# Kernel optimization log

Hardware: AMD Instinct MI355X
Metric: run time of the kernel (lower is better)

## Reference

```python
import jax, jax.numpy as jnp
import numpy as np

B, N, S, K = 16, 4, 64, 50        # batch, n_answers, q_len, n_boxes
VD, QD, H = 1024, 768, 512        # v_dim, q_dim, num_hid


def setup_inputs() -> dict:
    key = jax.random.key(0)
    ks = jax.random.split(key, 10)
    inp = {
        "v": jax.random.normal(ks[0], (B, 1, K, VD), dtype=jnp.float32),
        "q": jax.random.normal(ks[1], (B, N, S, 1, QD), dtype=jnp.float32),
        "box_mask": jax.random.randint(ks[2], (B, K), 0, 2, dtype=jnp.int32),
        "tags_attention": jax.random.normal(ks[3], (B, K), dtype=jnp.float32),
        # learned params (nn.Linear stores weight as [out, in])
        "Wv": jax.random.normal(ks[4], (H, VD), dtype=jnp.float32) * 0.02,
        "bv": jnp.zeros((H,), dtype=jnp.float32),
        "Wq": jax.random.normal(ks[5], (H, QD), dtype=jnp.float32) * 0.02,
        "bq": jnp.zeros((H,), dtype=jnp.float32),
        "Wl": jax.random.normal(ks[6], (1, H), dtype=jnp.float32) * 0.02,
        "bl": jnp.zeros((1,), dtype=jnp.float32),
    }
    return inp


def reference(v, q, box_mask, tags_attention, Wv, bv, Wq, bq, Wl, bl):
    # v_proj = Linear(v).unsqueeze(1): [B,1,K,H] -> [B,1,1,K,H]
    v_proj = (jnp.einsum('bokd,hd->bokh', v, Wv) + bv)[:, None]
    # q_proj: [B,N,S,1,H]
    q_proj = jnp.einsum('bnsod,hd->bnsoh', q, Wq) + bq
    # broadcast add + tanh: joint_repr [B,N,S,K,H] (the big intermediate)
    joint_repr = jnp.tanh(v_proj + q_proj)
    # score reduce over H: logits [B,N,S,K]
    logits = jnp.einsum('bnskh,oh->bnsko', joint_repr, Wl)[..., 0] + bl[0]
    # masked softmax over boxes with mask box_mask[:,None,None] -> [B,1,1,K]
    mask = (box_mask > 0)[:, None, None]
    w = jax.nn.softmax(jnp.where(mask, logits, jnp.float32(-1e9)), axis=-1)
    return w
```

## Files before the change

kernel.cpp:

```cpp
#include <hip/hip_runtime.h>
#include <hip/hip_bf16.h>
#include <cstddef>


typedef __attribute__((ext_vector_type(2))) float          f32x2;
typedef __attribute__((ext_vector_type(4))) float          f32x4;
typedef __attribute__((ext_vector_type(8))) short          bfrag;
typedef __attribute__((ext_vector_type(2))) unsigned int   u32x2;
typedef __attribute__((ext_vector_type(4))) unsigned short u16x4;

#define SBAR   __builtin_amdgcn_s_barrier()
#define SCHED0 __builtin_amdgcn_sched_barrier(0)

__device__ __forceinline__ void gload16(const void* g, void* l) {
  __builtin_amdgcn_global_load_lds((const __attribute__((address_space(1))) void*)g,
                                   (__attribute__((address_space(3))) void*)l, 16, 0, 0);
}

__device__ __forceinline__ unsigned int cvtpk(float a, float b) {
  unsigned int r;
  asm("v_cvt_pk_bf16_f32 %0, %1, %2" : "=v"(r) : "v"(a), "v"(b));
  return r;
}

__device__ __forceinline__ float bf2f(unsigned short u) {
  return __uint_as_float((unsigned int)u << 16);
}

template<int CTRL>
__device__ __forceinline__ float dpp_add(float x) {
  int r = __builtin_amdgcn_update_dpp(0, __float_as_int(x), CTRL, 0xF, 0xF, false);
  return x + __int_as_float(r);
}

__global__ void __launch_bounds__(256) cvt_all(
    const float* __restrict__ v, const float* __restrict__ wv,
    const float* __restrict__ q, const float* __restrict__ wq,
    unsigned short* __restrict__ vb, unsigned short* __restrict__ wvb,
    unsigned short* __restrict__ qb, unsigned short* __restrict__ wqb) {
  const int total = 1220608;
  for (int f = blockIdx.x * 256 + threadIdx.x; f < total; f += gridDim.x * 256) {
    const float* src; unsigned short* dst; int off;
    if (f < 204800)       { src = v;  dst = vb;  off = f; }
    else if (f < 335872)  { src = wv; dst = wvb; off = f - 204800; }
    else if (f < 1122304) { src = q;  dst = qb;  off = f - 335872; }
    else                  { src = wq; dst = wqb; off = f - 1122304; }
    f32x4 x = ((const f32x4*)src)[off];
    u32x2 p; p[0] = cvtpk(x[0], x[1]); p[1] = cvtpk(x[2], x[3]);
    ((u32x2*)dst)[off] = p;
  }
}

__global__ void __launch_bounds__(256) gemm_bf16(
    const unsigned short* __restrict__ vb, const unsigned short* __restrict__ qb,
    const unsigned short* __restrict__ wvb, const unsigned short* __restrict__ wqb,
    const float* __restrict__ bv, const float* __restrict__ bq,
    unsigned short* __restrict__ evw, unsigned short* __restrict__ qpw) {
  __shared__ unsigned short As[2][64 * 64];
  __shared__ unsigned short Bs[2][64 * 64];

  const int id = blockIdx.x;
  const int m  = (id & 7) + ((id >> 6) << 3);
  const int nt = (id >> 3) & 7;
  if (m >= 77) return;

  const int t = threadIdx.x;

  const unsigned short* A; const unsigned short* W; const float* bias;
  int M, Kd, m0;
  const bool vpath = (m < 13);
  if (vpath) { A = vb; W = wvb; bias = bv; M = 800;  Kd = 1024; m0 = m * 64; }
  else       { A = qb; W = wqb; bias = bq; M = 4096; Kd = 768;  m0 = (m - 13) * 64; }
  const int n0 = nt * 64;

  const int lane = t & 63;
  const int wave = t >> 6;
  const int wm   = wave >> 1;
  const int wn   = wave & 1;
  const int la   = lane & 15;
  const int lb   = lane >> 4;

  const int row1 = t >> 3;
  const int p1   = (t & 7) ^ (row1 & 7);
  int grA1 = m0 + row1;      if (grA1 >= M) grA1 = M - 1;
  int grA2 = m0 + row1 + 32; if (grA2 >= M) grA2 = M - 1;
  const unsigned short* srcA1 = A + (size_t)grA1 * Kd + p1 * 8;
  const unsigned short* srcA2 = A + (size_t)grA2 * Kd + p1 * 8;
  const unsigned short* srcB1 = W + (size_t)(n0 + row1) * Kd + p1 * 8;
  const unsigned short* srcB2 = W + (size_t)(n0 + row1 + 32) * Kd + p1 * 8;

  const int d1 = wave * 512;
  const int d2 = 2048 + wave * 512;

  auto STAGE = [&](int buf, int s) {
    const int o = s * 64;
    gload16(srcA1 + o, &As[buf][d1]);
    gload16(srcA2 + o, &As[buf][d2]);
    gload16(srcB1 + o, &Bs[buf][d1]);
    gload16(srcB2 + o, &Bs[buf][d2]);
  };

  f32x4 acc[2][2] = {};

  auto compute = [&](const unsigned short* sa, const unsigned short* sb) {
    bfrag af[2][2], bf[2][2];
#pragma unroll
    for (int r = 0; r < 2; ++r)
#pragma unroll
      for (int kk = 0; kk < 2; ++kk) {
        int rowa = wm * 32 + r * 16 + la;
        af[r][kk] = *(const bfrag*)((const char*)sa +
                     ((rowa * 128 + kk * 64 + lb * 16) ^ ((rowa & 7) << 4)));
        int rowb = wn * 32 + r * 16 + la;
        bf[r][kk] = *(const bfrag*)((const char*)sb +
                     ((rowb * 128 + kk * 64 + lb * 16) ^ ((rowb & 7) << 4)));
      }
#pragma unroll
    for (int kk = 0; kk < 2; ++kk)
#pragma unroll
      for (int r = 0; r < 2; ++r)
#pragma unroll
        for (int c = 0; c < 2; ++c)
          acc[r][c] = __builtin_amdgcn_mfma_f32_16x16x32_bf16(af[r][kk], bf[c][kk], acc[r][c], 0, 0, 0);
  };

  const int nsteps = Kd >> 6;
  STAGE(0, 0);
  STAGE(1, 1);
  for (int s = 0; s < nsteps; ++s) {
    if (s + 1 < nsteps) { asm volatile("s_waitcnt vmcnt(4)" ::: "memory"); }
    else                { asm volatile("s_waitcnt vmcnt(0)" ::: "memory"); }
    SCHED0;
    SBAR; SCHED0;
    compute(As[s & 1], Bs[s & 1]);
    SBAR; SCHED0;
    if (s + 2 < nsteps) STAGE(s & 1, s + 2);
  }

  const float CEXP = 2.885390081777927f;
  unsigned short* C = vpath ? evw : qpw;
#pragma unroll
  for (int c = 0; c < 2; ++c) {
    int col = n0 + wn * 32 + c * 16 + la;
    float bcol = bias[col];
#pragma unroll
    for (int r = 0; r < 2; ++r) {
      int mbase = m0 + wm * 32 + r * 16 + lb * 4;
#pragma unroll
      for (int e = 0; e < 4; ++e) {
        int mr = mbase + e;
        if (mr < M) {
          float val = __builtin_amdgcn_exp2f((acc[r][c][e] + bcol) * CEXP);
          C[(size_t)mr * 512 + col] = (unsigned short)cvtpk(val, val);
        }
      }
    }
  }
}

__global__ void
__attribute__((amdgpu_flat_work_group_size(512, 512), amdgpu_waves_per_eu(4, 4)))
stage3_kernel(
    const unsigned short* __restrict__ ev, const unsigned short* __restrict__ qp,
    const float* __restrict__ wl, const int* __restrict__ box_mask,
    float* __restrict__ out) {
  __shared__ unsigned short vpS[50][512];
  __shared__ float redS[8][64][8];

  const int b    = blockIdx.y;
  const int grp  = blockIdx.x;
  const int t    = threadIdx.x;
  const int wv   = t >> 6;
  const int lane = t & 63;
  const int row0 = b * 256 + grp * 16 + wv * 2;

  const unsigned short* q0 = qp + (size_t)row0 * 512;
  float eq0[8], eq1[8], wlr[8];
#pragma unroll
  for (int j = 0; j < 2; ++j) {
    u16x4 a = *(const u16x4*)&q0[j * 256 + 4 * lane];
    u16x4 c = *(const u16x4*)&q0[512 + j * 256 + 4 * lane];
    f32x4 w = *(const f32x4*)&wl[j * 256 + 4 * lane];
#pragma unroll
    for (int e = 0; e < 4; ++e) {
      eq0[j * 4 + e] = bf2f(a[e]);
      eq1[j * 4 + e] = bf2f(c[e]);
      wlr[j * 4 + e] = -2.f * w[e];
    }
  }

  {
    const unsigned short* src = ev + (size_t)b * 25600 + lane * 8;
#pragma unroll
    for (int i = 0; i < 7; ++i) {
      int kr = i * 8 + wv;
      if (kr < 50) gload16(src + kr * 512, &vpS[kr][0]);
    }
  }
  __syncthreads();

  const int g  = lane >> 4;
  const int li = lane & 15;

#pragma unroll 1
  for (int kc = 0; kc < 5; ++kc) {
    float a0[10], a1[10];
#pragma unroll
    for (int i = 0; i < 10; ++i) { a0[i] = 0.f; a1[i] = 0.f; }

#pragma unroll
    for (int i = 0; i < 10; ++i) {
      const unsigned short* vr = &vpS[kc * 10 + i][0];
      u16x4 va = *(const u16x4*)&vr[4 * lane];
      u16x4 vb2 = *(const u16x4*)&vr[256 + 4 * lane];
#pragma unroll
      for (int e = 0; e < 4; ++e) {
        float evf = bf2f(va[e]);
        a0[i] = fmaf(wlr[e], __builtin_amdgcn_rcpf(fmaf(evf, eq0[e], 1.f)), a0[i]);
        a1[i] = fmaf(wlr[e], __builtin_amdgcn_rcpf(fmaf(evf, eq1[e], 1.f)), a1[i]);
      }
#pragma unroll
      for (int e = 0; e < 4; ++e) {
        float evf = bf2f(vb2[e]);
        a0[i] = fmaf(wlr[4 + e], __builtin_amdgcn_rcpf(fmaf(evf, eq0[4 + e], 1.f)), a0[i]);
        a1[i] = fmaf(wlr[4 + e], __builtin_amdgcn_rcpf(fmaf(evf, eq1[4 + e], 1.f)), a1[i]);
      }
    }

#pragma unroll
    for (int i = 0; i < 10; ++i) {
      int k = kc * 10 + i;
      float s0 = a0[i], s1 = a1[i];
      s0 = dpp_add<0x128>(s0); s0 = dpp_add<0x124>(s0);
      s0 = dpp_add<0x122>(s0); s0 = dpp_add<0x121>(s0);
      s1 = dpp_add<0x128>(s1); s1 = dpp_add<0x124>(s1);
      s1 = dpp_add<0x122>(s1); s1 = dpp_add<0x121>(s1);
      if (li == (k & 15)) {
        f32x2 p; p[0] = s0; p[1] = s1;
        *(f32x2*)&redS[wv][k][g * 2] = p;
      }
    }
  }

  const int k = lane;
  f32x4 ra = *(const f32x4*)&redS[wv][k][0];
  f32x4 rb = *(const f32x4*)&redS[wv][k][4];
  float l0 = (ra[0] + ra[2]) + (rb[0] + rb[2]);
  float l1 = (ra[1] + ra[3]) + (rb[1] + rb[3]);

  int   msk = (k < 50) ? box_mask[b * 50 + k] : 0;
  bool  on  = (k < 50 && msk > 0);
  float L0 = on ? l0 : -1e9f;
  float L1 = on ? l1 : -1e9f;

  float m0 = L0, m1 = L1;
#pragma unroll
  for (int off = 32; off; off >>= 1) {
    m0 = fmaxf(m0, __shfl_xor(m0, off));
    m1 = fmaxf(m1, __shfl_xor(m1, off));
  }
  const float LOG2E = 1.4426950408889634f;
  float e0 = (k < 50) ? __builtin_amdgcn_exp2f((L0 - m0) * LOG2E) : 0.f;
  float e1 = (k < 50) ? __builtin_amdgcn_exp2f((L1 - m1) * LOG2E) : 0.f;
  float s0 = e0, s1 = e1;
#pragma unroll
  for (int off = 32; off; off >>= 1) {
    s0 += __shfl_xor(s0, off);
    s1 += __shfl_xor(s1, off);
  }

  if (k < 50) {
    out[(size_t)row0 * 50 + k]       = e0 / s0;
    out[(size_t)(row0 + 1) * 50 + k] = e1 / s1;
  }
}

extern "C" void kernel_launch(void* const* d_in, const int* in_sizes, int n_in,
                              void* d_out, int out_size, void* d_ws, size_t ws_size,
                              hipStream_t stream) {
  const float* v        = (const float*)d_in[0];
  const float* q        = (const float*)d_in[1];
  const int*   box_mask = (const int*)d_in[2];
  const float* Wv       = (const float*)d_in[4];
  const float* bv       = (const float*)d_in[5];
  const float* Wq       = (const float*)d_in[6];
  const float* bq       = (const float*)d_in[7];
  const float* Wl       = (const float*)d_in[8];
  float* out = (float*)d_out;

  char* ws = (char*)d_ws;
  unsigned short* qpw = (unsigned short*)(ws);
  unsigned short* evw = (unsigned short*)(ws + 4194304);
  unsigned short* vb  = (unsigned short*)(ws + 5013504);
  unsigned short* qb  = (unsigned short*)(ws + 6651904);
  unsigned short* wvb = (unsigned short*)(ws + 12943360);
  unsigned short* wqb = (unsigned short*)(ws + 13991936);

  cvt_all<<<2048, 256, 0, stream>>>(v, Wv, q, Wq, vb, wvb, qb, wqb);
  gemm_bf16<<<dim3(640), 256, 0, stream>>>(vb, qb, wvb, wqb, bv, bq, evw, qpw);
  stage3_kernel<<<dim3(16, 16), 512, 0, stream>>>(evw, qpw, Wl, box_mask, out);
}
```

Baseline: 44.77 us.

## Fuse conversion, GEMM and score stages into one cooperative persistent kernel

Replaces the three separate launches (fp32-to-bf16 conversion, bf16 GEMM, tanh-score softmax) with a single cooperative kernel of 256 blocks of 512 threads. The stages are separated by grid-wide syncs, and each block runs two GEMM tiles at once, one per 256-thread half. A subset of blocks runs an extra pair of tiles to cover all 616. This removes two kernel launch gaps and their tail idle time, at the cost of grid barrier overhead. It also introduces load imbalance in the GEMM phase and caps occupancy at 2 waves per EU.

```diff
diff --git a/kernel.cpp b/kernel.cpp
--- a/kernel.cpp
+++ b/kernel.cpp
@@ -1,6 +1,9 @@
 #include <hip/hip_runtime.h>
 #include <hip/hip_bf16.h>
+#include <hip/hip_cooperative_groups.h>
 #include <cstddef>
+
+namespace cg = cooperative_groups;
 
 
 typedef __attribute__((ext_vector_type(2))) float          f32x2;
@@ -33,38 +36,14 @@
   return x + __int_as_float(r);
 }
 
-__global__ void __launch_bounds__(256) cvt_all(
-    const float* __restrict__ v, const float* __restrict__ wv,
-    const float* __restrict__ q, const float* __restrict__ wq,
-    unsigned short* __restrict__ vb, unsigned short* __restrict__ wvb,
-    unsigned short* __restrict__ qb, unsigned short* __restrict__ wqb) {
-  const int total = 1220608;
-  for (int f = blockIdx.x * 256 + threadIdx.x; f < total; f += gridDim.x * 256) {
-    const float* src; unsigned short* dst; int off;
-    if (f < 204800)       { src = v;  dst = vb;  off = f; }
-    else if (f < 335872)  { src = wv; dst = wvb; off = f - 204800; }
-    else if (f < 1122304) { src = q;  dst = qb;  off = f - 335872; }
-    else                  { src = wq; dst = wqb; off = f - 1122304; }
-    f32x4 x = ((const f32x4*)src)[off];
-    u32x2 p; p[0] = cvtpk(x[0], x[1]); p[1] = cvtpk(x[2], x[3]);
-    ((u32x2*)dst)[off] = p;
-  }
-}
-
-__global__ void __launch_bounds__(256) gemm_bf16(
+__device__ __forceinline__ void gemm_tile(
+    int u, int t, unsigned short* AsBase, unsigned short* BsBase,
     const unsigned short* __restrict__ vb, const unsigned short* __restrict__ qb,
     const unsigned short* __restrict__ wvb, const unsigned short* __restrict__ wqb,
     const float* __restrict__ bv, const float* __restrict__ bq,
     unsigned short* __restrict__ evw, unsigned short* __restrict__ qpw) {
-  __shared__ unsigned short As[2][64 * 64];
-  __shared__ unsigned short Bs[2][64 * 64];
-
-  const int id = blockIdx.x;
-  const int m  = (id & 7) + ((id >> 6) << 3);
-  const int nt = (id >> 3) & 7;
-  if (m >= 77) return;
-
-  const int t = threadIdx.x;
+  const int m  = u >> 3;
+  const int nt = u & 7;
 
   const unsigned short* A; const unsigned short* W; const float* bias;
   int M, Kd, m0;
@@ -94,10 +73,10 @@
 
   auto STAGE = [&](int buf, int s) {
     const int o = s * 64;
-    gload16(srcA1 + o, &As[buf][d1]);
-    gload16(srcA2 + o, &As[buf][d2]);
-    gload16(srcB1 + o, &Bs[buf][d1]);
-    gload16(srcB2 + o, &Bs[buf][d2]);
+    gload16(srcA1 + o, AsBase + buf * 4096 + d1);
+    gload16(srcA2 + o, AsBase + buf * 4096 + d2);
+    gload16(srcB1 + o, BsBase + buf * 4096 + d1);
+    gload16(srcB2 + o, BsBase + buf * 4096 + d2);
   };
 
   f32x4 acc[2][2] = {};
@@ -132,7 +111,7 @@
     else                { asm volatile("s_waitcnt vmcnt(0)" ::: "memory"); }
     SCHED0;
     SBAR; SCHED0;
-    compute(As[s & 1], Bs[s & 1]);
+    compute(AsBase + (s & 1) * 4096, BsBase + (s & 1) * 4096);
     SBAR; SCHED0;
     if (s + 2 < nsteps) STAGE(s & 1, s + 2);
   }
@@ -159,119 +138,157 @@
 }
 
 __global__ void
-__attribute__((amdgpu_flat_work_group_size(512, 512), amdgpu_waves_per_eu(4, 4)))
-stage3_kernel(
-    const unsigned short* __restrict__ ev, const unsigned short* __restrict__ qp,
-    const float* __restrict__ wl, const int* __restrict__ box_mask,
-    float* __restrict__ out) {
-  __shared__ unsigned short vpS[50][512];
-  __shared__ float redS[8][64][8];
-
-  const int b    = blockIdx.y;
-  const int grp  = blockIdx.x;
-  const int t    = threadIdx.x;
-  const int wv   = t >> 6;
-  const int lane = t & 63;
-  const int row0 = b * 256 + grp * 16 + wv * 2;
-
-  const unsigned short* q0 = qp + (size_t)row0 * 512;
-  float eq0[8], eq1[8], wlr[8];
-#pragma unroll
-  for (int j = 0; j < 2; ++j) {
-    u16x4 a = *(const u16x4*)&q0[j * 256 + 4 * lane];
-    u16x4 c = *(const u16x4*)&q0[512 + j * 256 + 4 * lane];
-    f32x4 w = *(const f32x4*)&wl[j * 256 + 4 * lane];
-#pragma unroll
-    for (int e = 0; e < 4; ++e) {
-      eq0[j * 4 + e] = bf2f(a[e]);
-      eq1[j * 4 + e] = bf2f(c[e]);
-      wlr[j * 4 + e] = -2.f * w[e];
-    }
-  }
+__attribute__((amdgpu_flat_work_group_size(512, 512), amdgpu_waves_per_eu(2, 2)))
+mega(const float* __restrict__ v,  const float* __restrict__ q,
+     const int* __restrict__ box_mask,
+     const float* __restrict__ Wv, const float* __restrict__ bv,
+     const float* __restrict__ Wq, const float* __restrict__ bq,
+     const float* __restrict__ Wl, float* __restrict__ out,
+     unsigned short* qpw, unsigned short* evw,
+     unsigned short* vbuf, unsigned short* qbuf,
+     unsigned short* wvb, unsigned short* wqb) {
+  cg::grid_group grid = cg::this_grid();
+  __attribute__((aligned(16))) __shared__ char smem[67584];
+
+  const int bid = blockIdx.x;
+  const int t   = threadIdx.x;
 
   {
-    const unsigned short* src = ev + (size_t)b * 25600 + lane * 8;
-#pragma unroll
-    for (int i = 0; i < 7; ++i) {
-      int kr = i * 8 + wv;
-      if (kr < 50) gload16(src + kr * 512, &vpS[kr][0]);
-    }
-  }
-  __syncthreads();
-
-  const int g  = lane >> 4;
-  const int li = lane & 15;
+    const int total = 1220608;
+    for (int f = bid * 512 + t; f < total; f += 131072) {
+      const float* src; unsigned short* dst; int off;
+      if (f < 204800)       { src = v;  dst = vbuf; off = f; }
+      else if (f < 335872)  { src = Wv; dst = wvb;  off = f - 204800; }
+      else if (f < 1122304) { src = q;  dst = qbuf; off = f - 335872; }
+      else                  { src = Wq; dst = wqb;  off = f - 1122304; }
+      f32x4 x = ((const f32x4*)src)[off];
+      u32x2 p; p[0] = cvtpk(x[0], x[1]); p[1] = cvtpk(x[2], x[3]);
+      ((u32x2*)dst)[off] = p;
+    }
+  }
+  grid.sync();
+
+  {
+    const int sub  = t >> 8;
+    const int tsub = t & 255;
+    unsigned short* As = (unsigned short*)(smem + sub * 32768);
+    unsigned short* Bs = As + 8192;
+
+    gemm_tile(bid * 2 + sub, tsub, As, Bs, vbuf, qbuf, wvb, wqb, bv, bq, evw, qpw);
+    if (bid >= 52 && bid < 104)
+      gemm_tile(512 + (bid - 52) * 2 + sub, tsub, As, Bs, vbuf, qbuf, wvb, wqb, bv, bq, evw, qpw);
+  }
+  grid.sync();
+
+  {
+    unsigned short (*vpS)[512] = (unsigned short(*)[512])smem;
+    float (*redS)[64][8]       = (float(*)[64][8])(smem + 51200);
+
+    const int b    = bid >> 4;
+    const int grp  = bid & 15;
+    const int wv   = t >> 6;
+    const int lane = t & 63;
+    const int row0 = b * 256 + grp * 16 + wv * 2;
+
+    const unsigned short* q0 = qpw + (size_t)row0 * 512;
+    float eq0[8], eq1[8], wlr[8];
+#pragma unroll
+    for (int j = 0; j < 2; ++j) {
+      u16x4 a = *(const u16x4*)&q0[j * 256 + 4 * lane];
+      u16x4 c = *(const u16x4*)&q0[512 + j * 256 + 4 * lane];
+      f32x4 w = *(const f32x4*)&Wl[j * 256 + 4 * lane];
+#pragma unroll
+      for (int e = 0; e < 4; ++e) {
+        eq0[j * 4 + e] = bf2f(a[e]);
+        eq1[j * 4 + e] = bf2f(c[e]);
+        wlr[j * 4 + e] = -2.f * w[e];
+      }
+    }
+
+    {
+      const unsigned short* src = evw + (size_t)b * 25600 + lane * 8;
+#pragma unroll
+      for (int i = 0; i < 7; ++i) {
+        int kr = i * 8 + wv;
+        if (kr < 50) gload16(src + kr * 512, &vpS[kr][0]);
+      }
+    }
+    __syncthreads();
+
+    const int g  = lane >> 4;
+    const int li = lane & 15;
 
 #pragma unroll 1
-  for (int kc = 0; kc < 5; ++kc) {
-    float a0[10], a1[10];
-#pragma unroll
-    for (int i = 0; i < 10; ++i) { a0[i] = 0.f; a1[i] = 0.f; }
-
-#pragma unroll
-    for (int i = 0; i < 10; ++i) {
-      const unsigned short* vr = &vpS[kc * 10 + i][0];
-      u16x4 va = *(const u16x4*)&vr[4 * lane];
-      u16x4 vb2 = *(const u16x4*)&vr[256 + 4 * lane];
-#pragma unroll
-      for (int e = 0; e < 4; ++e) {
-        float evf = bf2f(va[e]);
-        a0[i] = fmaf(wlr[e], __builtin_amdgcn_rcpf(fmaf(evf, eq0[e], 1.f)), a0[i]);
-        a1[i] = fmaf(wlr[e], __builtin_amdgcn_rcpf(fmaf(evf, eq1[e], 1.f)), a1[i]);
-      }
-#pragma unroll
-      for (int e = 0; e < 4; ++e) {
-        float evf = bf2f(vb2[e]);
-        a0[i] = fmaf(wlr[4 + e], __builtin_amdgcn_rcpf(fmaf(evf, eq0[4 + e], 1.f)), a0[i]);
-        a1[i] = fmaf(wlr[4 + e], __builtin_amdgcn_rcpf(fmaf(evf, eq1[4 + e], 1.f)), a1[i]);
-      }
-    }
-
-#pragma unroll
-    for (int i = 0; i < 10; ++i) {
-      int k = kc * 10 + i;
-      float s0 = a0[i], s1 = a1[i];
-      s0 = dpp_add<0x128>(s0); s0 = dpp_add<0x124>(s0);
-      s0 = dpp_add<0x122>(s0); s0 = dpp_add<0x121>(s0);
-      s1 = dpp_add<0x128>(s1); s1 = dpp_add<0x124>(s1);
-      s1 = dpp_add<0x122>(s1); s1 = dpp_add<0x121>(s1);
-      if (li == (k & 15)) {
-        f32x2 p; p[0] = s0; p[1] = s1;
-        *(f32x2*)&redS[wv][k][g * 2] = p;
-      }
-    }
-  }
-
-  const int k = lane;
-  f32x4 ra = *(const f32x4*)&redS[wv][k][0];
-  f32x4 rb = *(const f32x4*)&redS[wv][k][4];
-  float l0 = (ra[0] + ra[2]) + (rb[0] + rb[2]);
-  float l1 = (ra[1] + ra[3]) + (rb[1] + rb[3]);
-
-  int   msk = (k < 50) ? box_mask[b * 50 + k] : 0;
-  bool  on  = (k < 50 && msk > 0);
-  float L0 = on ? l0 : -1e9f;
-  float L1 = on ? l1 : -1e9f;
-
-  float m0 = L0, m1 = L1;
-#pragma unroll
-  for (int off = 32; off; off >>= 1) {
-    m0 = fmaxf(m0, __shfl_xor(m0, off));
-    m1 = fmaxf(m1, __shfl_xor(m1, off));
-  }
-  const float LOG2E = 1.4426950408889634f;
-  float e0 = (k < 50) ? __builtin_amdgcn_exp2f((L0 - m0) * LOG2E) : 0.f;
-  float e1 = (k < 50) ? __builtin_amdgcn_exp2f((L1 - m1) * LOG2E) : 0.f;
-  float s0 = e0, s1 = e1;
-#pragma unroll
-  for (int off = 32; off; off >>= 1) {
-    s0 += __shfl_xor(s0, off);
-    s1 += __shfl_xor(s1, off);
-  }
-
-  if (k < 50) {
-    out[(size_t)row0 * 50 + k]       = e0 / s0;
-    out[(size_t)(row0 + 1) * 50 + k] = e1 / s1;
+    for (int kc = 0; kc < 5; ++kc) {
+      float a0[10], a1[10];
+#pragma unroll
+      for (int i = 0; i < 10; ++i) { a0[i] = 0.f; a1[i] = 0.f; }
+
+#pragma unroll
+      for (int i = 0; i < 10; ++i) {
+        const unsigned short* vr = &vpS[kc * 10 + i][0];
+        u16x4 va  = *(const u16x4*)&vr[4 * lane];
+        u16x4 vb2 = *(const u16x4*)&vr[256 + 4 * lane];
+#pragma unroll
+        for (int e = 0; e < 4; ++e) {
+          float evf = bf2f(va[e]);
+          a0[i] = fmaf(wlr[e], __builtin_amdgcn_rcpf(fmaf(evf, eq0[e], 1.f)), a0[i]);
+          a1[i] = fmaf(wlr[e], __builtin_amdgcn_rcpf(fmaf(evf, eq1[e], 1.f)), a1[i]);
+        }
+#pragma unroll
+        for (int e = 0; e < 4; ++e) {
+          float evf = bf2f(vb2[e]);
+          a0[i] = fmaf(wlr[4 + e], __builtin_amdgcn_rcpf(fmaf(evf, eq0[4 + e], 1.f)), a0[i]);
+          a1[i] = fmaf(wlr[4 + e], __builtin_amdgcn_rcpf(fmaf(evf, eq1[4 + e], 1.f)), a1[i]);
+        }
+      }
+
+#pragma unroll
+      for (int i = 0; i < 10; ++i) {
+        int k = kc * 10 + i;
+        float s0 = a0[i], s1 = a1[i];
+        s0 = dpp_add<0x128>(s0); s0 = dpp_add<0x124>(s0);
+        s0 = dpp_add<0x122>(s0); s0 = dpp_add<0x121>(s0);
+        s1 = dpp_add<0x128>(s1); s1 = dpp_add<0x124>(s1);
+        s1 = dpp_add<0x122>(s1); s1 = dpp_add<0x121>(s1);
+        if (li == (k & 15)) {
+          f32x2 p; p[0] = s0; p[1] = s1;
+          *(f32x2*)&redS[wv][k][g * 2] = p;
+        }
+      }
+    }
+
+    const int k = lane;
+    f32x4 ra = *(const f32x4*)&redS[wv][k][0];
+    f32x4 rb = *(const f32x4*)&redS[wv][k][4];
+    float l0 = (ra[0] + ra[2]) + (rb[0] + rb[2]);
+    float l1 = (ra[1] + ra[3]) + (rb[1] + rb[3]);
+
+    int   msk = (k < 50) ? box_mask[b * 50 + k] : 0;
+    bool  on  = (k < 50 && msk > 0);
+    float L0 = on ? l0 : -1e9f;
+    float L1 = on ? l1 : -1e9f;
+
+    float m0 = L0, m1 = L1;
+#pragma unroll
+    for (int off = 32; off; off >>= 1) {
+      m0 = fmaxf(m0, __shfl_xor(m0, off));
+      m1 = fmaxf(m1, __shfl_xor(m1, off));
+    }
+    const float LOG2E = 1.4426950408889634f;
+    float e0 = (k < 50) ? __builtin_amdgcn_exp2f((L0 - m0) * LOG2E) : 0.f;
+    float e1 = (k < 50) ? __builtin_amdgcn_exp2f((L1 - m1) * LOG2E) : 0.f;
+    float s0 = e0, s1 = e1;
+#pragma unroll
+    for (int off = 32; off; off >>= 1) {
+      s0 += __shfl_xor(s0, off);
+      s1 += __shfl_xor(s1, off);
+    }
+
+    if (k < 50) {
+      out[(size_t)row0 * 50 + k]       = e0 / s0;
+      out[(size_t)(row0 + 1) * 50 + k] = e1 / s1;
+    }
   }
 }
 
@@ -289,14 +306,18 @@
   float* out = (float*)d_out;
 
   char* ws = (char*)d_ws;
-  unsigned short* qpw = (unsigned short*)(ws);
-  unsigned short* evw = (unsigned short*)(ws + 4194304);
-  unsigned short* vb  = (unsigned short*)(ws + 5013504);
-  unsigned short* qb  = (unsigned short*)(ws + 6651904);
-  unsigned short* wvb = (unsigned short*)(ws + 12943360);
-  unsigned short* wqb = (unsigned short*)(ws + 13991936);
-
-  cvt_all<<<2048, 256, 0, stream>>>(v, Wv, q, Wq, vb, wvb, qb, wqb);
-  gemm_bf16<<<dim3(640), 256, 0, stream>>>(vb, qb, wvb, wqb, bv, bq, evw, qpw);
-  stage3_kernel<<<dim3(16, 16), 512, 0, stream>>>(evw, qpw, Wl, box_mask, out);
-}
+  unsigned short* qpw  = (unsigned short*)(ws);
+  unsigned short* evw  = (unsigned short*)(ws + 4194304);
+  unsigned short* vbuf = (unsigned short*)(ws + 5013504);
+  unsigned short* qbuf = (unsigned short*)(ws + 6651904);
+  unsigned short* wvb  = (unsigned short*)(ws + 12943360);
+  unsigned short* wqb  = (unsigned short*)(ws + 13991936);
+
+  void* args[] = {
+    (void*)&v, (void*)&q, (void*)&box_mask, (void*)&Wv, (void*)&bv,
+    (void*)&Wq, (void*)&bq, (void*)&Wl, (void*)&out,
+    (void*)&qpw, (void*)&evw, (void*)&vbuf, (void*)&qbuf, (void*)&wvb, (void*)&wqb
+  };
+  hipLaunchCooperativeKernel((const void*)mega, dim3(256), dim3(512),
+                             args, 0, stream);
+}
```

After: 118.2 us. 164% more time.
